# Kernel tuning notes

Measured on AMD Instinct MI355X. Metric: run time of the kernel, lower is better.

Reference implementation:

```python
import jax, jax.numpy as jnp
import numpy as np

N_NODES = 100000
N_EDGES = 1600000
IN_DIM = 128
HIDDEN = [128, 128]
MLP_HIDDEN = [64]


def _glorot(key, shape):
    fan_in, fan_out = shape[0], shape[1]
    s = jnp.sqrt(6.0 / (fan_in + fan_out))
    return jax.random.uniform(key, shape, jnp.float32, -s, s)


def setup_inputs() -> dict:
    key = jax.random.key(0)
    ks = jax.random.split(key, 16)
    x = jax.random.normal(ks[0], (N_NODES, IN_DIM), jnp.float32)
    edge_weight = jax.random.uniform(ks[1], (N_EDGES,), jnp.float32)
    edge_src = jax.random.randint(ks[2], (N_EDGES,), 0, N_NODES, jnp.int32)
    edge_dst = jax.random.randint(ks[3], (N_EDGES,), 0, N_NODES, jnp.int32)
    # GraphConvolution layer params
    W1 = _glorot(ks[4], (IN_DIM, HIDDEN[0]))
    b1 = jnp.zeros((HIDDEN[0],), jnp.float32)
    W2 = _glorot(ks[5], (HIDDEN[0], HIDDEN[1]))
    b2 = jnp.zeros((HIDDEN[1],), jnp.float32)
    # tau head MLP: rep_dim -> 64 -> 1
    tw1 = _glorot(ks[6], (HIDDEN[1], MLP_HIDDEN[0]))
    tb1 = jnp.zeros((MLP_HIDDEN[0],), jnp.float32)
    tw2 = _glorot(ks[7], (MLP_HIDDEN[0], 1))
    tb2 = jnp.zeros((1,), jnp.float32)
    # propensity head: rep_dim -> 1, sigmoid
    pw = _glorot(ks[8], (HIDDEN[1], 1))
    pb = jnp.zeros((1,), jnp.float32)
    return {"x": x, "edge_weight": edge_weight, "W1": W1, "b1": b1, "W2": W2, "b2": b2,
            "tw1": tw1, "tb1": tb1, "tw2": tw2, "tb2": tb2, "pw": pw, "pb": pb,
            "edge_src": edge_src, "edge_dst": edge_dst}


def _gcn_layer(h, W, b, edge_src, edge_dst, edge_weight):
    # GraphConvolution: support = h @ W; out = spmm(adj, support) + b
    support = h @ W                                   # [N, H]
    msg = support[edge_src] * edge_weight[:, None]    # [E, H] gather + scale
    agg = jax.ops.segment_sum(msg, edge_dst, num_segments=N_NODES)  # [N, H]
    return agg + b


def reference(x, edge_weight, W1, b1, W2, b2, tw1, tb1, tw2, tb2, pw, pb, edge_src, edge_dst):
    h = jax.nn.relu(_gcn_layer(x, W1, b1, edge_src, edge_dst, edge_weight))
    h = jax.nn.relu(_gcn_layer(h, W2, b2, edge_src, edge_dst, edge_weight))
    rep = h                                            # [N, rep_dim]
    tau_pred = (jax.nn.relu(rep @ tw1 + tb1) @ tw2 + tb2)[:, 0]  # [N]
    e = jax.nn.sigmoid(rep @ pw + pb)[:, 0]            # [N]
    return tau_pred, e, rep
```

## Files before the change

kernel.cpp:

```cpp
#include <hip/hip_runtime.h>
#include <hip/hip_bf16.h>
#include <math.h>


#define PSZ 128
#define BIN_CH 16384

typedef __attribute__((ext_vector_type(8))) short bfrag;
typedef __attribute__((ext_vector_type(4))) float ffrag;

static __device__ __forceinline__ ushort f2bf(float f) {
    __hip_bfloat16 h = __float2bfloat16(f);
    return *reinterpret_cast<ushort*>(&h);
}
static __device__ __forceinline__ float bf2f(ushort u) {
    __hip_bfloat16 h;
    *reinterpret_cast<ushort*>(&h) = u;
    return __bfloat162float(h);
}


__global__ __launch_bounds__(256) void k_bhist(const int* __restrict__ edst,
                                               int* __restrict__ bcnt,
                                               int nE, int NB) {
    extern __shared__ int h[];
    const int tid = threadIdx.x;
    const int e0  = blockIdx.x * BIN_CH;
    for (int b = tid; b < NB; b += 256) h[b] = 0;
    __syncthreads();
    for (int i = tid; i < BIN_CH; i += 256) {
        int e = e0 + i;
        if (e < nE) atomicAdd(&h[edst[e] >> 7], 1);
    }
    __syncthreads();
    for (int b = tid; b < NB; b += 256) {
        int v = h[b];
        if (v) atomicAdd(&bcnt[b], v);
    }
}

__global__ __launch_bounds__(1024) void k_bscan(const int* __restrict__ bcnt,
                                                int* __restrict__ bof,
                                                int* __restrict__ gcur,
                                                int NB, int nE) {
    __shared__ int s[1024];
    const int t = threadIdx.x;
    const int v = (t < NB) ? bcnt[t] : 0;
    s[t] = v; __syncthreads();
    for (int o = 1; o < 1024; o <<= 1) {
        int u = (t >= o) ? s[t - o] : 0;
        __syncthreads(); s[t] += u; __syncthreads();
    }
    if (t < NB) { int ex = s[t] - v; bof[t] = ex; gcur[t] = ex; }
    if (t == 0) bof[NB] = nE;
}

__global__ __launch_bounds__(256) void k_bin(const int* __restrict__ edst,
                                             const int* __restrict__ esrc,
                                             const float* __restrict__ ew,
                                             int* __restrict__ gcur,
                                             unsigned int* __restrict__ pkbin,
                                             unsigned char* __restrict__ dlbin,
                                             int nE, int NB) {
    extern __shared__ int sm[];
    int* hcnt  = sm;
    int* hbase = sm + NB;
    int* hcur  = sm + 2 * NB;
    const int tid = threadIdx.x;
    const int e0  = blockIdx.x * BIN_CH;

    for (int b = tid; b < NB; b += 256) hcnt[b] = 0;
    __syncthreads();
    for (int i = tid; i < BIN_CH; i += 256) {
        int e = e0 + i;
        if (e < nE) atomicAdd(&hcnt[edst[e] >> 7], 1);
    }
    __syncthreads();
    for (int b = tid; b < NB; b += 256) {
        int c = hcnt[b];
        hbase[b] = c ? atomicAdd(&gcur[b], c) : 0;
        hcur[b] = 0;
    }
    __syncthreads();
    for (int i = tid; i < BIN_CH; i += 256) {
        int e = e0 + i;
        if (e < nE) {
            int d = edst[e];
            int p = d >> 7;
            int pos = atomicAdd(&hcur[p], 1);
            int idx = hbase[p] + pos;
            unsigned int w15 = (unsigned int)rintf(ew[e] * 32767.0f);
            pkbin[idx] = (w15 << 17) | (unsigned int)esrc[e];
            dlbin[idx] = (unsigned char)(d & 127);
        }
    }
}

__global__ __launch_bounds__(256) void k_placepart(
    const unsigned int* __restrict__ pkbin, const unsigned char* __restrict__ dlbin,
    const int* __restrict__ bof, int* __restrict__ off,
    unsigned int* __restrict__ spack, int nN, int NB)
{
    __shared__ int lcnt[PSZ];
    __shared__ int lexc[PSZ];
    const int tid  = threadIdx.x;
    const int p    = blockIdx.x;
    const int base = bof[p];
    const int tot  = bof[p + 1] - base;

    if (tid < PSZ) lcnt[tid] = 0;
    __syncthreads();
    for (int i = tid; i < tot; i += 256)
        atomicAdd(&lcnt[dlbin[base + i]], 1);
    __syncthreads();
    if (tid < PSZ) lexc[tid] = lcnt[tid];
    __syncthreads();
    for (int o = 1; o < PSZ; o <<= 1) {
        int u = 0;
        if (tid < PSZ && tid >= o) u = lexc[tid - o];
        __syncthreads();
        if (tid < PSZ) lexc[tid] += u;
        __syncthreads();
    }
    if (tid < PSZ) {
        lexc[tid] -= lcnt[tid];
        int gd = p * PSZ + tid;
        if (gd < nN) off[gd] = base + lexc[tid];
        lcnt[tid] = 0;
    }
    if (p == NB - 1 && tid == 0) off[nN] = base + tot;
    __syncthreads();
    for (int i = tid; i < tot; i += 256) {
        unsigned int pk = pkbin[base + i];
        int dl = dlbin[base + i];
        int r = atomicAdd(&lcnt[dl], 1);
        spack[base + lexc[dl] + r] = pk;
    }
}

__global__ __launch_bounds__(256) void k_prepW(const float* __restrict__ W1,
                                               const float* __restrict__ W2,
                                               ushort* __restrict__ Wt1,
                                               ushort* __restrict__ Wt2) {
    const float* W  = (blockIdx.x == 0) ? W1 : W2;
    ushort*      Wt = (blockIdx.x == 0) ? Wt1 : Wt2;
    for (int j = 0; j < 64; ++j) {
        int idx = threadIdx.x + j * 256;
        int k = idx >> 7, n = idx & 127;
        Wt[n * 128 + k] = f2bf(W[idx]);
    }
}

template <int ABF16>
__global__ __launch_bounds__(256) void gemm_mfma(
    const void* __restrict__ Av, const ushort* __restrict__ Wt,
    ushort* __restrict__ Y, int nN)
{
    __shared__ ushort Xl[64 * 128];
    __shared__ ushort Wl[128 * 128];
    const int tid  = threadIdx.x;
    const int row0 = blockIdx.x * 64;

    if (ABF16) {
        const int4* X16 = (const int4*)Av;
        #pragma unroll
        for (int j = 0; j < 4; ++j) {
            int u  = tid + j * 256;
            int r  = u >> 4;
            int cb = (u & 15) * 16;
            int grow = row0 + r;
            int4 v = make_int4(0, 0, 0, 0);
            if (grow < nN) v = X16[(size_t)grow * 16 + (u & 15)];
            *(int4*)((char*)Xl + r * 256 + (cb ^ ((r & 7) << 4))) = v;
        }
    } else {
        const float4* X4 = (const float4*)Av;
        #pragma unroll
        for (int j = 0; j < 8; ++j) {
            int u  = tid + j * 256;
            int r  = u >> 5;
            int c4 = (u & 31) * 4;
            int grow = row0 + r;
            float4 v = make_float4(0.f, 0.f, 0.f, 0.f);
            if (grow < nN) v = X4[(size_t)grow * 32 + (u & 31)];
            ushort4 o;
            o.x = f2bf(v.x); o.y = f2bf(v.y); o.z = f2bf(v.z); o.w = f2bf(v.w);
            *(ushort4*)((char*)Xl + r * 256 + ((c4 * 2) ^ ((r & 7) << 4))) = o;
        }
    }
    {
        const int4* Wg = (const int4*)Wt;
        #pragma unroll
        for (int j = 0; j < 8; ++j) {
            int u  = tid + j * 256;
            int r  = u >> 4;
            int cb = (u & 15) * 16;
            *(int4*)((char*)Wl + r * 256 + (cb ^ ((r & 7) << 4))) = Wg[u];
        }
    }
    __syncthreads();

    const int lane = tid & 63;
    const int wid  = tid >> 6;
    const int wrow = wid * 16;
    const int arow = wrow + (lane & 15);
    const int kg16 = (lane >> 4) * 16;

    ffrag acc[8];
    #pragma unroll
    for (int ct = 0; ct < 8; ++ct) acc[ct] = (ffrag){0.f, 0.f, 0.f, 0.f};

    #pragma unroll
    for (int ks = 0; ks < 4; ++ks) {
        const int abyte = arow * 256 + ((ks * 64 + kg16) ^ ((arow & 7) << 4));
        bfrag a = *(const bfrag*)((const char*)Xl + abyte);
        #pragma unroll
        for (int ct = 0; ct < 8; ++ct) {
            const int wcol = ct * 16 + (lane & 15);
            const int bbyte = wcol * 256 + ((ks * 64 + kg16) ^ ((wcol & 7) << 4));
            bfrag b = *(const bfrag*)((const char*)Wl + bbyte);
            acc[ct] = __builtin_amdgcn_mfma_f32_16x16x32_bf16(a, b, acc[ct], 0, 0, 0);
        }
    }

    #pragma unroll
    for (int ct = 0; ct < 8; ++ct) {
        #pragma unroll
        for (int i = 0; i < 4; ++i) {
            int row = row0 + wrow + (lane >> 4) * 4 + i;
            if (row < nN)
                Y[(size_t)row * 128 + ct * 16 + (lane & 15)] = f2bf(acc[ct][i]);
        }
    }
}

template <int EPHASE, int OUTBF>
__global__ __launch_bounds__(256) void k_agg_half(
    const ushort* __restrict__ S, const unsigned int* __restrict__ spack,
    const int* __restrict__ off, const float* __restrict__ bias,
    void* __restrict__ out, const float* __restrict__ pw,
    const float* __restrict__ pb, float* __restrict__ out_e,
    int nN, int half)
{
    const int g      = (blockIdx.x * 256 + threadIdx.x) >> 4;
    const int lane16 = threadIdx.x & 15;
    if (g >= nN) return;
    const int c  = half * 64 + lane16 * 4;
    const int j0 = off[g], j1 = off[g + 1];

    float4 acc = make_float4(0.f, 0.f, 0.f, 0.f);
    const float wscale = 1.0f / 32767.0f;

    int j = j0;
    for (; j + 8 <= j1; j += 8) {
        unsigned int p[8];
        #pragma unroll
        for (int q = 0; q < 8; ++q) p[q] = spack[j + q];
        ushort4 v[8];
        #pragma unroll
        for (int q = 0; q < 8; ++q)
            v[q] = *(const ushort4*)&S[(size_t)(p[q] & 0x1FFFF) * 128 + c];
        #pragma unroll
        for (int q = 0; q < 8; ++q) {
            const float w = (float)(p[q] >> 17) * wscale;
            acc.x = fmaf(bf2f(v[q].x), w, acc.x);
            acc.y = fmaf(bf2f(v[q].y), w, acc.y);
            acc.z = fmaf(bf2f(v[q].z), w, acc.z);
            acc.w = fmaf(bf2f(v[q].w), w, acc.w);
        }
    }
    for (; j < j1; ++j) {
        const unsigned int p = spack[j];
        const float w = (float)(p >> 17) * wscale;
        const ushort4 v = *(const ushort4*)&S[(size_t)(p & 0x1FFFF) * 128 + c];
        acc.x = fmaf(bf2f(v.x), w, acc.x);
        acc.y = fmaf(bf2f(v.y), w, acc.y);
        acc.z = fmaf(bf2f(v.z), w, acc.z);
        acc.w = fmaf(bf2f(v.w), w, acc.w);
    }

    const float4 bb = ((const float4*)bias)[half * 16 + lane16];
    acc.x = fmaxf(acc.x + bb.x, 0.f);
    acc.y = fmaxf(acc.y + bb.y, 0.f);
    acc.z = fmaxf(acc.z + bb.z, 0.f);
    acc.w = fmaxf(acc.w + bb.w, 0.f);

    if (OUTBF) {
        ushort4 o;
        o.x = f2bf(acc.x); o.y = f2bf(acc.y); o.z = f2bf(acc.z); o.w = f2bf(acc.w);
        *(ushort4*)&((ushort*)out)[(size_t)g * 128 + c] = o;
    } else {
        *(float4*)&((float*)out)[(size_t)g * 128 + c] = acc;
    }

    if (EPHASE) {
        const float4 pv = ((const float4*)pw)[half * 16 + lane16];
        float ep = acc.x * pv.x + acc.y * pv.y + acc.z * pv.z + acc.w * pv.w;
        #pragma unroll
        for (int o = 1; o < 16; o <<= 1) ep += __shfl_xor(ep, o);
        if (lane16 == 0) {
            if (EPHASE == 1) out_e[g] = ep;
            else out_e[g] = 1.f / (1.f + expf(-(ep + out_e[g] + pb[0])));
        }
    }
}

__global__ __launch_bounds__(256) void tau_kernel(
    const float* __restrict__ REP, const float* __restrict__ tw1,
    const float* __restrict__ tb1, const float* __restrict__ tw2,
    const float* __restrict__ tb2, float* __restrict__ out_tau, int nN)
{
    __shared__ float Rl[64 * 132];
    __shared__ float Wl[64 * 64];
    __shared__ float stb1[64], stw2[64];

    const int tid  = threadIdx.x;
    const int row0 = blockIdx.x * 64;

    if (tid < 64) { stb1[tid] = tb1[tid]; stw2[tid] = tw2[tid]; }

    #pragma unroll
    for (int j = 0; j < 8; ++j) {
        int i  = tid + j * 256;
        int r  = i >> 5;
        int c4 = i & 31;
        float4 v = make_float4(0.f, 0.f, 0.f, 0.f);
        if (row0 + r < nN) v = ((const float4*)REP)[(size_t)(row0 + r) * 32 + c4];
        ((float4*)Rl)[r * 33 + c4] = v;
    }

    const int cg = tid & 15;
    const int rt = tid >> 4;

    float4 acc[4];
    #pragma unroll
    for (int r = 0; r < 4; ++r) acc[r] = make_float4(0.f, 0.f, 0.f, 0.f);

    for (int kc = 0; kc < 2; ++kc) {
        __syncthreads();
        {
            const float4* s4 = (const float4*)tw1 + kc * 1024;
            #pragma unroll
            for (int j = 0; j < 4; ++j)
                ((float4*)Wl)[tid + j * 256] = s4[tid + j * 256];
        }
        __syncthreads();
        #pragma unroll
        for (int k4 = 0; k4 < 16; ++k4) {
            float4 xr[4];
            #pragma unroll
            for (int r = 0; r < 4; ++r)
                xr[r] = *(const float4*)&Rl[(rt * 4 + r) * 132 + kc * 64 + k4 * 4];
            #pragma unroll
            for (int kk = 0; kk < 4; ++kk) {
                float4 w = *(const float4*)&Wl[(k4 * 4 + kk) * 64 + cg * 4];
                #pragma unroll
                for (int r = 0; r < 4; ++r) {
                    float xv = (kk == 0) ? xr[r].x : (kk == 1) ? xr[r].y
                             : (kk == 2) ? xr[r].z : xr[r].w;
                    acc[r].x = fmaf(xv, w.x, acc[r].x);
                    acc[r].y = fmaf(xv, w.y, acc[r].y);
                    acc[r].z = fmaf(xv, w.z, acc[r].z);
                    acc[r].w = fmaf(xv, w.w, acc[r].w);
                }
            }
        }
    }

    const float4 tb = *(const float4*)&stb1[cg * 4];
    const float4 t2 = *(const float4*)&stw2[cg * 4];
    float taup[4];
    #pragma unroll
    for (int r = 0; r < 4; ++r) {
        float hx = fmaxf(acc[r].x + tb.x, 0.f);
        float hy = fmaxf(acc[r].y + tb.y, 0.f);
        float hz = fmaxf(acc[r].z + tb.z, 0.f);
        float hw = fmaxf(acc[r].w + tb.w, 0.f);
        taup[r] = hx * t2.x + hy * t2.y + hz * t2.z + hw * t2.w;
    }
    #pragma unroll
    for (int o = 1; o < 16; o <<= 1) {
        #pragma unroll
        for (int r = 0; r < 4; ++r) taup[r] += __shfl_xor(taup[r], o);
    }
    if (cg == 0) {
        const float tb2v = tb2[0];
        #pragma unroll
        for (int r = 0; r < 4; ++r) {
            int row = row0 + rt * 4 + r;
            if (row < nN) out_tau[row] = taup[r] + tb2v;
        }
    }
}

extern "C" void kernel_launch(void* const* d_in, const int* in_sizes, int n_in,
                              void* d_out, int out_size, void* d_ws, size_t ws_size,
                              hipStream_t stream)
{
    const float* x   = (const float*)d_in[0];
    const float* ew  = (const float*)d_in[1];
    const float* W1  = (const float*)d_in[2];
    const float* b1  = (const float*)d_in[3];
    const float* W2  = (const float*)d_in[4];
    const float* b2  = (const float*)d_in[5];
    const float* tw1 = (const float*)d_in[6];
    const float* tb1 = (const float*)d_in[7];
    const float* tw2 = (const float*)d_in[8];
    const float* tb2 = (const float*)d_in[9];
    const float* pw  = (const float*)d_in[10];
    const float* pb  = (const float*)d_in[11];
    const int* esrc  = (const int*)d_in[12];
    const int* edst  = (const int*)d_in[13];

    const int nN = in_sizes[0] / 128;
    const int nE = in_sizes[1];
    const int NB = (nN + PSZ - 1) / PSZ;

    char* w = (char*)d_ws;
    ushort*        S     = (ushort*)w;         w += (size_t)nN * 128 * 2;
    ushort*        Bh    = (ushort*)w;         w += (size_t)nN * 128 * 2;
    unsigned int*  spack = (unsigned int*)w;   w += (size_t)nE * 4;
    unsigned int*  pkbin = (unsigned int*)w;   w += (size_t)nE * 4;
    unsigned char* dlbin = (unsigned char*)w;  w += (size_t)nE;
    ushort*        Wt1   = (ushort*)w;         w += 16384 * 2;
    ushort*        Wt2   = (ushort*)w;         w += 16384 * 2;
    int*           off   = (int*)w;            w += (size_t)(nN + 1) * 4;
    int*           bcnt  = (int*)w;            w += (size_t)NB * 4;
    int*           bof   = (int*)w;            w += (size_t)(NB + 1) * 4;
    int*           gcur  = (int*)w;            w += (size_t)NB * 4;

    float* out_tau = (float*)d_out;
    float* out_e   = out_tau + nN;
    float* out_rep = out_e + nN;

    const int binBlocks  = (nE + BIN_CH - 1) / BIN_CH;
    const int gemmBlocks = (nN + 63) / 64;
    const int aggBlocks  = (nN + 15) / 16;
    const int tauBlocks  = (nN + 63) / 64;
    const size_t histLds = (size_t)NB * sizeof(int);

    hipMemsetAsync(bcnt, 0, (size_t)NB * sizeof(int), stream);
    k_bhist<<<binBlocks, 256, histLds, stream>>>(edst, bcnt, nE, NB);
    k_bscan<<<1, 1024, 0, stream>>>(bcnt, bof, gcur, NB, nE);
    k_bin<<<binBlocks, 256, 3 * histLds, stream>>>(edst, esrc, ew, gcur,
                                                   pkbin, dlbin, nE, NB);
    k_placepart<<<NB, 256, 0, stream>>>(pkbin, dlbin, bof, off, spack, nN, NB);

    k_prepW<<<2, 256, 0, stream>>>(W1, W2, Wt1, Wt2);

    gemm_mfma<0><<<gemmBlocks, 256, 0, stream>>>(x, Wt1, S, nN);
    k_agg_half<0, 1><<<aggBlocks, 256, 0, stream>>>(S, spack, off, b1, Bh,
                                                    nullptr, nullptr, nullptr, nN, 0);
    k_agg_half<0, 1><<<aggBlocks, 256, 0, stream>>>(S, spack, off, b1, Bh,
                                                    nullptr, nullptr, nullptr, nN, 1);

    gemm_mfma<1><<<gemmBlocks, 256, 0, stream>>>(Bh, Wt2, S, nN);
    k_agg_half<1, 0><<<aggBlocks, 256, 0, stream>>>(S, spack, off, b2, out_rep,
                                                    pw, pb, out_e, nN, 0);
    k_agg_half<2, 0><<<aggBlocks, 256, 0, stream>>>(S, spack, off, b2, out_rep,
                                                    pw, pb, out_e, nN, 1);

    tau_kernel<<<tauBlocks, 256, 0, stream>>>(out_rep, tw1, tb1, tw2, tb2,
                                              out_tau, nN);
}
```

Before: 347.4 us.

## Pack dst-local into edge word, merge agg halves, read W directly

Edge weights are quantized from 15 to 8 bits so that the destination-local index fits in the packed edge word, which removes the separate dlbin byte array and its traffic. Each of the two aggregation passes per layer, previously split into two column halves, becomes a single kernel with 32 lanes per node, so the edge list is read once instead of twice and the propensity output is computed in one pass. The GEMM reads weight fragments straight from global memory instead of staging them in LDS. Histogram and binning chunk sizes are also reduced to raise the number of blocks. The 8-bit weight quantization gives up accuracy and risks exceeding tolerance, and merging the halves means a larger gather footprint per node in each pass.

```diff
diff --git a/kernel.cpp b/kernel.cpp
--- a/kernel.cpp
+++ b/kernel.cpp
@@ -4,7 +4,8 @@
 
 
 #define PSZ 128
-#define BIN_CH 16384
+#define BH_CH 2048
+#define BIN_CH 4096
 
 typedef __attribute__((ext_vector_type(8))) short bfrag;
 typedef __attribute__((ext_vector_type(4))) float ffrag;
@@ -25,10 +26,10 @@
                                                int nE, int NB) {
     extern __shared__ int h[];
     const int tid = threadIdx.x;
-    const int e0  = blockIdx.x * BIN_CH;
+    const int e0  = blockIdx.x * BH_CH;
     for (int b = tid; b < NB; b += 256) h[b] = 0;
     __syncthreads();
-    for (int i = tid; i < BIN_CH; i += 256) {
+    for (int i = tid; i < BH_CH; i += 256) {
         int e = e0 + i;
         if (e < nE) atomicAdd(&h[edst[e] >> 7], 1);
     }
@@ -60,7 +61,6 @@
                                              const float* __restrict__ ew,
                                              int* __restrict__ gcur,
                                              unsigned int* __restrict__ pkbin,
-                                             unsigned char* __restrict__ dlbin,
                                              int nE, int NB) {
     extern __shared__ int sm[];
     int* hcnt  = sm;
@@ -77,8 +77,8 @@
     }
     __syncthreads();
     for (int b = tid; b < NB; b += 256) {
-        int c = hcnt[b];
-        hbase[b] = c ? atomicAdd(&gcur[b], c) : 0;
+        int cv = hcnt[b];
+        hbase[b] = cv ? atomicAdd(&gcur[b], cv) : 0;
         hcur[b] = 0;
     }
     __syncthreads();
@@ -88,18 +88,16 @@
             int d = edst[e];
             int p = d >> 7;
             int pos = atomicAdd(&hcur[p], 1);
-            int idx = hbase[p] + pos;
-            unsigned int w15 = (unsigned int)rintf(ew[e] * 32767.0f);
-            pkbin[idx] = (w15 << 17) | (unsigned int)esrc[e];
-            dlbin[idx] = (unsigned char)(d & 127);
+            unsigned int w8 = (unsigned int)rintf(ew[e] * 255.0f);
+            pkbin[hbase[p] + pos] =
+                (w8 << 24) | ((unsigned int)(d & 127) << 17) | (unsigned int)esrc[e];
         }
     }
 }
 
 __global__ __launch_bounds__(256) void k_placepart(
-    const unsigned int* __restrict__ pkbin, const unsigned char* __restrict__ dlbin,
-    const int* __restrict__ bof, int* __restrict__ off,
-    unsigned int* __restrict__ spack, int nN, int NB)
+    const unsigned int* __restrict__ pkbin, const int* __restrict__ bof,
+    int* __restrict__ off, unsigned int* __restrict__ spack, int nN, int NB)
 {
     __shared__ int lcnt[PSZ];
     __shared__ int lexc[PSZ];
@@ -111,7 +109,7 @@
     if (tid < PSZ) lcnt[tid] = 0;
     __syncthreads();
     for (int i = tid; i < tot; i += 256)
-        atomicAdd(&lcnt[dlbin[base + i]], 1);
+        atomicAdd(&lcnt[(pkbin[base + i] >> 17) & 127], 1);
     __syncthreads();
     if (tid < PSZ) lexc[tid] = lcnt[tid];
     __syncthreads();
@@ -132,7 +130,7 @@
     __syncthreads();
     for (int i = tid; i < tot; i += 256) {
         unsigned int pk = pkbin[base + i];
-        int dl = dlbin[base + i];
+        int dl = (pk >> 17) & 127;
         int r = atomicAdd(&lcnt[dl], 1);
         spack[base + lexc[dl] + r] = pk;
     }
@@ -157,7 +155,6 @@
     ushort* __restrict__ Y, int nN)
 {
     __shared__ ushort Xl[64 * 128];
-    __shared__ ushort Wl[128 * 128];
     const int tid  = threadIdx.x;
     const int row0 = blockIdx.x * 64;
 
@@ -188,16 +185,6 @@
             *(ushort4*)((char*)Xl + r * 256 + ((c4 * 2) ^ ((r & 7) << 4))) = o;
         }
     }
-    {
-        const int4* Wg = (const int4*)Wt;
-        #pragma unroll
-        for (int j = 0; j < 8; ++j) {
-            int u  = tid + j * 256;
-            int r  = u >> 4;
-            int cb = (u & 15) * 16;
-            *(int4*)((char*)Wl + r * 256 + (cb ^ ((r & 7) << 4))) = Wg[u];
-        }
-    }
     __syncthreads();
 
     const int lane = tid & 63;
@@ -217,8 +204,7 @@
         #pragma unroll
         for (int ct = 0; ct < 8; ++ct) {
             const int wcol = ct * 16 + (lane & 15);
-            const int bbyte = wcol * 256 + ((ks * 64 + kg16) ^ ((wcol & 7) << 4));
-            bfrag b = *(const bfrag*)((const char*)Wl + bbyte);
+            bfrag b = *(const bfrag*)(Wt + wcol * 128 + ks * 32 + (lane >> 4) * 8);
             acc[ct] = __builtin_amdgcn_mfma_f32_16x16x32_bf16(a, b, acc[ct], 0, 0, 0);
         }
     }
@@ -234,22 +220,21 @@
     }
 }
 
-template <int EPHASE, int OUTBF>
-__global__ __launch_bounds__(256) void k_agg_half(
+template <int EP, int OUTBF>
+__global__ __launch_bounds__(256) void k_aggregate(
     const ushort* __restrict__ S, const unsigned int* __restrict__ spack,
     const int* __restrict__ off, const float* __restrict__ bias,
     void* __restrict__ out, const float* __restrict__ pw,
-    const float* __restrict__ pb, float* __restrict__ out_e,
-    int nN, int half)
+    const float* __restrict__ pb, float* __restrict__ out_e, int nN)
 {
-    const int g      = (blockIdx.x * 256 + threadIdx.x) >> 4;
-    const int lane16 = threadIdx.x & 15;
+    const int g    = (blockIdx.x * 256 + threadIdx.x) >> 5;
+    const int lane = threadIdx.x & 31;
     if (g >= nN) return;
-    const int c  = half * 64 + lane16 * 4;
+    const int c  = lane * 4;
     const int j0 = off[g], j1 = off[g + 1];
 
     float4 acc = make_float4(0.f, 0.f, 0.f, 0.f);
-    const float wscale = 1.0f / 32767.0f;
+    const float wscale = 1.0f / 255.0f;
 
     int j = j0;
     for (; j + 8 <= j1; j += 8) {
@@ -262,7 +247,7 @@
             v[q] = *(const ushort4*)&S[(size_t)(p[q] & 0x1FFFF) * 128 + c];
         #pragma unroll
         for (int q = 0; q < 8; ++q) {
-            const float w = (float)(p[q] >> 17) * wscale;
+            const float w = (float)(p[q] >> 24) * wscale;
             acc.x = fmaf(bf2f(v[q].x), w, acc.x);
             acc.y = fmaf(bf2f(v[q].y), w, acc.y);
             acc.z = fmaf(bf2f(v[q].z), w, acc.z);
@@ -271,7 +256,7 @@
     }
     for (; j < j1; ++j) {
         const unsigned int p = spack[j];
-        const float w = (float)(p >> 17) * wscale;
+        const float w = (float)(p >> 24) * wscale;
         const ushort4 v = *(const ushort4*)&S[(size_t)(p & 0x1FFFF) * 128 + c];
         acc.x = fmaf(bf2f(v.x), w, acc.x);
         acc.y = fmaf(bf2f(v.y), w, acc.y);
@@ -279,7 +264,7 @@
         acc.w = fmaf(bf2f(v.w), w, acc.w);
     }
 
-    const float4 bb = ((const float4*)bias)[half * 16 + lane16];
+    const float4 bb = ((const float4*)bias)[lane];
     acc.x = fmaxf(acc.x + bb.x, 0.f);
     acc.y = fmaxf(acc.y + bb.y, 0.f);
     acc.z = fmaxf(acc.z + bb.z, 0.f);
@@ -293,15 +278,12 @@
         *(float4*)&((float*)out)[(size_t)g * 128 + c] = acc;
     }
 
-    if (EPHASE) {
-        const float4 pv = ((const float4*)pw)[half * 16 + lane16];
+    if (EP) {
+        const float4 pv = ((const float4*)pw)[lane];
         float ep = acc.x * pv.x + acc.y * pv.y + acc.z * pv.z + acc.w * pv.w;
         #pragma unroll
-        for (int o = 1; o < 16; o <<= 1) ep += __shfl_xor(ep, o);
-        if (lane16 == 0) {
-            if (EPHASE == 1) out_e[g] = ep;
-            else out_e[g] = 1.f / (1.f + expf(-(ep + out_e[g] + pb[0])));
-        }
+        for (int o = 1; o < 32; o <<= 1) ep += __shfl_xor(ep, o);
+        if (lane == 0) out_e[g] = 1.f / (1.f + expf(-(ep + pb[0])));
     }
 }
 
@@ -417,48 +399,44 @@
     const int NB = (nN + PSZ - 1) / PSZ;
 
     char* w = (char*)d_ws;
-    ushort*        S     = (ushort*)w;         w += (size_t)nN * 128 * 2;
-    ushort*        Bh    = (ushort*)w;         w += (size_t)nN * 128 * 2;
-    unsigned int*  spack = (unsigned int*)w;   w += (size_t)nE * 4;
-    unsigned int*  pkbin = (unsigned int*)w;   w += (size_t)nE * 4;
-    unsigned char* dlbin = (unsigned char*)w;  w += (size_t)nE;
-    ushort*        Wt1   = (ushort*)w;         w += 16384 * 2;
-    ushort*        Wt2   = (ushort*)w;         w += 16384 * 2;
-    int*           off   = (int*)w;            w += (size_t)(nN + 1) * 4;
-    int*           bcnt  = (int*)w;            w += (size_t)NB * 4;
-    int*           bof   = (int*)w;            w += (size_t)(NB + 1) * 4;
-    int*           gcur  = (int*)w;            w += (size_t)NB * 4;
+    ushort*       S     = (ushort*)w;        w += (size_t)nN * 128 * 2;
+    ushort*       Bh    = (ushort*)w;        w += (size_t)nN * 128 * 2;
+    unsigned int* spack = (unsigned int*)w;  w += (size_t)nE * 4;
+    unsigned int* pkbin = (unsigned int*)w;  w += (size_t)nE * 4;
+    ushort*       Wt1   = (ushort*)w;        w += 16384 * 2;
+    ushort*       Wt2   = (ushort*)w;        w += 16384 * 2;
+    int*          off   = (int*)w;           w += (size_t)(nN + 1) * 4;
+    int*          bcnt  = (int*)w;           w += (size_t)NB * 4;
+    int*          bof   = (int*)w;           w += (size_t)(NB + 1) * 4;
+    int*          gcur  = (int*)w;           w += (size_t)NB * 4;
 
     float* out_tau = (float*)d_out;
     float* out_e   = out_tau + nN;
     float* out_rep = out_e + nN;
 
-    const int binBlocks  = (nE + BIN_CH - 1) / BIN_CH;
-    const int gemmBlocks = (nN + 63) / 64;
-    const int aggBlocks  = (nN + 15) / 16;
-    const int tauBlocks  = (nN + 63) / 64;
-    const size_t histLds = (size_t)NB * sizeof(int);
+    const int bhistBlocks = (nE + BH_CH - 1) / BH_CH;
+    const int binBlocks   = (nE + BIN_CH - 1) / BIN_CH;
+    const int gemmBlocks  = (nN + 63) / 64;
+    const int aggBlocks   = (nN + 7) / 8;
+    const int tauBlocks   = (nN + 63) / 64;
+    const size_t histLds  = (size_t)NB * sizeof(int);
 
     hipMemsetAsync(bcnt, 0, (size_t)NB * sizeof(int), stream);
-    k_bhist<<<binBlocks, 256, histLds, stream>>>(edst, bcnt, nE, NB);
+    k_bhist<<<bhistBlocks, 256, histLds, stream>>>(edst, bcnt, nE, NB);
     k_bscan<<<1, 1024, 0, stream>>>(bcnt, bof, gcur, NB, nE);
     k_bin<<<binBlocks, 256, 3 * histLds, stream>>>(edst, esrc, ew, gcur,
-                                                   pkbin, dlbin, nE, NB);
-    k_placepart<<<NB, 256, 0, stream>>>(pkbin, dlbin, bof, off, spack, nN, NB);
+                                                   pkbin, nE, NB);
+    k_placepart<<<NB, 256, 0, stream>>>(pkbin, bof, off, spack, nN, NB);
 
     k_prepW<<<2, 256, 0, stream>>>(W1, W2, Wt1, Wt2);
 
     gemm_mfma<0><<<gemmBlocks, 256, 0, stream>>>(x, Wt1, S, nN);
-    k_agg_half<0, 1><<<aggBlocks, 256, 0, stream>>>(S, spack, off, b1, Bh,
-                                                    nullptr, nullptr, nullptr, nN, 0);
-    k_agg_half<0, 1><<<aggBlocks, 256, 0, stream>>>(S, spack, off, b1, Bh,
-                                                    nullptr, nullptr, nullptr, nN, 1);
+    k_aggregate<0, 1><<<aggBlocks, 256, 0, stream>>>(S, spack, off, b1, Bh,
+                                                     nullptr, nullptr, nullptr, nN);
 
     gemm_mfma<1><<<gemmBlocks, 256, 0, stream>>>(Bh, Wt2, S, nN);
-    k_agg_half<1, 0><<<aggBlocks, 256, 0, stream>>>(S, spack, off, b2, out_rep,
-                                                    pw, pb, out_e, nN, 0);
-    k_agg_half<2, 0><<<aggBlocks, 256, 0, stream>>>(S, spack, off, b2, out_rep,
-                                                    pw, pb, out_e, nN, 1);
+    k_aggregate<1, 0><<<aggBlocks, 256, 0, stream>>>(S, spack, off, b2, out_rep,
+                                                     pw, pb, out_e, nN);
 
     tau_kernel<<<tauBlocks, 256, 0, stream>>>(out_rep, tw1, tb1, tw2, tb2,
                                               out_tau, nN);
```

New measurement: 339.1 us. -2.4%, faster.
